# Kernel tuning notes

Hardware: AMD Instinct MI355X
Metric: run time of the kernel (lower is better)

Reference implementation:

```python
import jax, jax.numpy as jnp
import numpy as np

N_ATOMS = 50000
N_EDGES = 640000
D = 128
N_RBF = 20
N_INTER = 3

act = jax.nn.softplus


def setup_inputs() -> dict:
    key = jax.random.key(0)
    ks = jax.random.split(key, 16)
    s = 1.0 / np.sqrt(D)
    inp = {
        "x": jax.random.normal(ks[0], (N_ATOMS, D), jnp.float32),
        "g_ij": jax.random.uniform(ks[1], (N_EDGES, N_RBF), jnp.float32),
        "idx_i": jax.random.randint(ks[2], (N_EDGES,), 0, N_ATOMS),
        "idx_j": jax.random.randint(ks[3], (N_EDGES,), 0, N_ATOMS),
        "n_atoms": N_ATOMS,
        "u": jnp.ones((D,), jnp.float32),
        "Wf": jax.random.normal(ks[4], (D, D), jnp.float32) * s,
        "bf": jnp.zeros((D,), jnp.float32),
        # linear_g weight init to zero in original; use small random so grads flow
        "Wg": jax.random.normal(ks[5], (D, N_RBF), jnp.float32) * 0.01,
        "bg": jnp.zeros((D,), jnp.float32),
        "Wj": jax.random.normal(ks[6], (D, D), jnp.float32) * s,
        "bj": jnp.zeros((D,), jnp.float32),
        "Wi": jax.random.normal(ks[7], (D, D), jnp.float32) * s,
        "bi": jnp.zeros((D,), jnp.float32),
        "res_w1": jax.random.normal(ks[8], (N_INTER, D, D), jnp.float32) * s,
        "res_b1": jnp.zeros((N_INTER, D), jnp.float32),
        "res_w2": jax.random.normal(ks[9], (N_INTER, D, D), jnp.float32) * s,
        "res_b2": jnp.zeros((N_INTER, D), jnp.float32),
    }
    return inp


def reference(x, g_ij, idx_i, idx_j, n_atoms, u, Wf, bf, Wg, bg, Wj, bj, Wi, bi,
              res_w1, res_b1, res_w2, res_b2):
    x_j = x[idx_j]                                    # [E, D] gather
    xp = u * x                                        # [N, D]
    # sequential_j: act -> linear_j -> act, gated by linear_g(g_ij)
    vp = act(act(x_j) @ Wj.T + bj) * (g_ij @ Wg.T + bg)   # [E, D]
    vm = act(act(x) @ Wi.T + bi)                      # [N, D]
    v = jax.ops.segment_sum(vp, idx_i, num_segments=n_atoms) + vm
    for l in range(res_w1.shape[0]):
        h = act(v) @ res_w1[l].T + res_b1[l]
        h = act(h) @ res_w2[l].T + res_b2[l]
        v = h + v
    v = act(v)
    return xp + v @ Wf.T + bf
```

## Files before the change

kernel.cpp:

```cpp
#include <hip/hip_runtime.h>
#include <hip/hip_fp16.h>

#define DD 128

typedef __attribute__((ext_vector_type(8))) short short8;
typedef __attribute__((ext_vector_type(8))) unsigned short ushort8;
typedef __attribute__((ext_vector_type(4))) float floatx4;
typedef unsigned int uint32;

__device__ __forceinline__ float sp(float x) {
    return fmaxf(x, 0.0f) + __logf(1.0f + __expf(-fabsf(x)));
}

__device__ __forceinline__ unsigned short f2bf(float f) {
    union { float f; uint32 u; } c; c.f = f;
    const uint32 u = c.u;
    return (unsigned short)((u + 0x7fffu + ((u >> 16) & 1u)) >> 16);
}

__device__ __forceinline__ unsigned short f2h(float f) {
    __half h = __float2half(f);
    return __builtin_bit_cast(unsigned short, h);
}

__global__ __launch_bounds__(256)
void convert_w(const float* __restrict__ Wj, const float* __restrict__ Wi,
               const float* __restrict__ rw1, const float* __restrict__ rw2,
               const float* __restrict__ Wf, unsigned short* __restrict__ out,
               const float* __restrict__ g, unsigned short* __restrict__ gh,
               int gchunks)
{
    if ((int)blockIdx.x >= 72) {
        const int gid = ((int)blockIdx.x - 72) * 256 + threadIdx.x;
        if (gid < gchunks) {
            const float4 f0 = reinterpret_cast<const float4*>(g)[2 * gid];
            const float4 f1 = reinterpret_cast<const float4*>(g)[2 * gid + 1];
            ushort8 o;
            o[0] = f2h(f0.x); o[1] = f2h(f0.y); o[2] = f2h(f0.z); o[3] = f2h(f0.w);
            o[4] = f2h(f1.x); o[5] = f2h(f1.y); o[6] = f2h(f1.z); o[7] = f2h(f1.w);
            reinterpret_cast<ushort8*>(gh)[gid] = o;
        }
        return;
    }
    const int gid = blockIdx.x * 256 + threadIdx.x;
    const int mat = gid >> 11;
    const int f8  = gid & 2047;
    const float* src;
    if      (mat == 0) src = Wj;
    else if (mat == 1) src = Wi;
    else if (mat <= 4) src = rw1 + (size_t)(mat - 2) * 16384;
    else if (mat <= 7) src = rw2 + (size_t)(mat - 5) * 16384;
    else               src = Wf;
    const int row = f8 >> 4;
    const int ch  = f8 & 15;
    const float4 a = reinterpret_cast<const float4*>(src)[2 * f8];
    const float4 b = reinterpret_cast<const float4*>(src)[2 * f8 + 1];
    ushort8 u8;
    u8[0] = f2bf(a.x); u8[1] = f2bf(a.y); u8[2] = f2bf(a.z); u8[3] = f2bf(a.w);
    u8[4] = f2bf(b.x); u8[5] = f2bf(b.y); u8[6] = f2bf(b.z); u8[7] = f2bf(b.w);
    *reinterpret_cast<ushort8*>(out + (size_t)mat * 16384 + row * 128 +
                                ((ch ^ (row & 15)) << 3)) = u8;
}

__device__ __forceinline__ void stage_wb(const unsigned short* __restrict__ Wb,
                                         unsigned short* wl, int t)
{
    #pragma unroll
    for (int i = 0; i < 8; ++i) {
        const int c = t + i * 256;
        *reinterpret_cast<ushort8*>(wl + c * 8) =
            *reinterpret_cast<const ushort8*>(Wb + c * 8);
    }
}

__device__ __forceinline__ void load_afrag_act(const float* __restrict__ X,
                                               int m, int q, int n, short8 af[4])
{
    const int mm = m < n ? m : n - 1;
    const float* row = X + (size_t)mm * DD + q * 8;
    #pragma unroll
    for (int kk = 0; kk < 4; ++kk) {
        const float4 a = *reinterpret_cast<const float4*>(row + kk * 32);
        const float4 b = *reinterpret_cast<const float4*>(row + kk * 32 + 4);
        ushort8 u;
        u[0] = f2bf(sp(a.x)); u[1] = f2bf(sp(a.y)); u[2] = f2bf(sp(a.z)); u[3] = f2bf(sp(a.w));
        u[4] = f2bf(sp(b.x)); u[5] = f2bf(sp(b.y)); u[6] = f2bf(sp(b.z)); u[7] = f2bf(sp(b.w));
        af[kk] = __builtin_bit_cast(short8, u);
    }
}

__device__ __forceinline__ void mfma_gemm(const unsigned short* wl,
                                          const short8 af[4],
                                          int cl, int q, floatx4 acc[8])
{
    #pragma unroll
    for (int nt = 0; nt < 8; ++nt) {
        const int nrow = nt * 16 + cl;
        #pragma unroll
        for (int kk = 0; kk < 4; ++kk) {
            const int chs = (kk * 4 + q) ^ cl;
            const short8 bfr = *reinterpret_cast<const short8*>(wl + nrow * 128 + (chs << 3));
            acc[nt] = __builtin_amdgcn_mfma_f32_16x16x32_bf16(af[kk], bfr, acc[nt], 0, 0, 0);
        }
    }
}

__global__ __launch_bounds__(256, 4)
void dual_gemm(const float* __restrict__ x,
               const unsigned short* __restrict__ Wb,
               const float* __restrict__ bj, const float* __restrict__ bi,
               unsigned short* __restrict__ Aout, float* __restrict__ vout, int n)
{
    __shared__ __align__(16) unsigned short wl[128 * 128];
    const int t = threadIdx.x;
    const int lane = t & 63, wv = t >> 6;
    const int cl = lane & 15, q = lane >> 4;
    const int m0 = blockIdx.x * 64 + wv * 16;

    short8 af[4];
    load_afrag_act(x, m0 + cl, q, n, af);

    stage_wb(Wb, wl, t);
    __syncthreads();

    floatx4 acc[8];
    #pragma unroll
    for (int nt = 0; nt < 8; ++nt) acc[nt] = (floatx4){0.f, 0.f, 0.f, 0.f};
    mfma_gemm(wl, af, cl, q, acc);

    #pragma unroll
    for (int nt = 0; nt < 8; ++nt) {
        const int col = nt * 16 + cl;
        const float bb = bj[col];
        #pragma unroll
        for (int r = 0; r < 4; ++r) {
            const int row = m0 + q * 4 + r;
            if (row < n) Aout[(size_t)row * DD + col] = f2bf(sp(acc[nt][r] + bb));
        }
    }

    __syncthreads();
    stage_wb(Wb + 16384, wl, t);
    __syncthreads();

    #pragma unroll
    for (int nt = 0; nt < 8; ++nt) acc[nt] = (floatx4){0.f, 0.f, 0.f, 0.f};
    mfma_gemm(wl, af, cl, q, acc);

    #pragma unroll
    for (int nt = 0; nt < 8; ++nt) {
        const int col = nt * 16 + cl;
        const float bb = bi[col];
        #pragma unroll
        for (int r = 0; r < 4; ++r) {
            const int row = m0 + q * 4 + r;
            if (row < n) vout[(size_t)row * DD + col] = sp(acc[nt][r] + bb);
        }
    }
}

__global__ __launch_bounds__(256, 2)
void tail_kernel(const float* __restrict__ vin, const float* __restrict__ x,
                 const unsigned short* __restrict__ Wb,
                 const float* __restrict__ rb1, const float* __restrict__ rb2,
                 const float* __restrict__ bf, const float* __restrict__ u,
                 float* __restrict__ out, int n)
{
    __shared__ __align__(16) unsigned short wl[2][128 * 128];
    __shared__ __align__(16) unsigned short hl[64 * 128];
    const int t = threadIdx.x;
    const int lane = t & 63, wv = t >> 6;
    const int cl = lane & 15, q = lane >> 4;
    const int mb = blockIdx.x * 64;
    const int ml2 = wv * 16 + cl;

    floatx4 vac[8];
    #pragma unroll
    for (int nt = 0; nt < 8; ++nt) {
        #pragma unroll
        for (int r = 0; r < 4; ++r) {
            const int row = mb + wv * 16 + q * 4 + r;
            const int col = nt * 16 + cl;
            vac[nt][r] = (row < n) ? vin[(size_t)row * DD + col] : 0.f;
        }
    }

    short8 af[4];
    load_afrag_act(vin, mb + wv * 16 + cl, q, n, af);

    stage_wb(Wb + 2 * 16384, wl[0], t);
    __syncthreads();
    int buf = 0;

    #pragma unroll
    for (int l = 0; l < 3; ++l) {
        stage_wb(Wb + (size_t)(5 + l) * 16384, wl[buf ^ 1], t);

        if (l > 0) {
            #pragma unroll
            for (int nt = 0; nt < 8; ++nt) {
                const int col = nt * 16 + cl;
                const int ch = col >> 3;
                #pragma unroll
                for (int r = 0; r < 4; ++r) {
                    const int ml = wv * 16 + q * 4 + r;
                    hl[ml * 128 + ((ch ^ (ml & 15)) << 3) + (col & 7)] = f2bf(sp(vac[nt][r]));
                }
            }
            #pragma unroll
            for (int kk = 0; kk < 4; ++kk)
                af[kk] = *reinterpret_cast<const short8*>(hl + ml2 * 128 + (((kk * 4 + q) ^ cl) << 3));
        }

        floatx4 acc[8];
        #pragma unroll
        for (int nt = 0; nt < 8; ++nt) acc[nt] = (floatx4){0.f, 0.f, 0.f, 0.f};
        mfma_gemm(wl[buf], af, cl, q, acc);

        const float* b1 = rb1 + (size_t)l * DD;
        #pragma unroll
        for (int nt = 0; nt < 8; ++nt) {
            const int col = nt * 16 + cl;
            const int ch = col >> 3;
            const float bb = b1[col];
            #pragma unroll
            for (int r = 0; r < 4; ++r) {
                const int ml = wv * 16 + q * 4 + r;
                hl[ml * 128 + ((ch ^ (ml & 15)) << 3) + (col & 7)] = f2bf(sp(acc[nt][r] + bb));
            }
        }
        short8 af2[4];
        #pragma unroll
        for (int kk = 0; kk < 4; ++kk)
            af2[kk] = *reinterpret_cast<const short8*>(hl + ml2 * 128 + (((kk * 4 + q) ^ cl) << 3));

        __syncthreads();
        buf ^= 1;

        const int nxt = (l < 2) ? (3 + l) : 8;
        stage_wb(Wb + (size_t)nxt * 16384, wl[buf ^ 1], t);

        mfma_gemm(wl[buf], af2, cl, q, vac);
        const float* b2 = rb2 + (size_t)l * DD;
        #pragma unroll
        for (int nt = 0; nt < 8; ++nt) {
            const float bb = b2[nt * 16 + cl];
            #pragma unroll
            for (int r = 0; r < 4; ++r) vac[nt][r] += bb;
        }

        __syncthreads();
        buf ^= 1;
    }

    #pragma unroll
    for (int nt = 0; nt < 8; ++nt) {
        const int col = nt * 16 + cl;
        const int ch = col >> 3;
        #pragma unroll
        for (int r = 0; r < 4; ++r) {
            const int ml = wv * 16 + q * 4 + r;
            hl[ml * 128 + ((ch ^ (ml & 15)) << 3) + (col & 7)] = f2bf(sp(vac[nt][r]));
        }
    }
    short8 aff[4];
    #pragma unroll
    for (int kk = 0; kk < 4; ++kk)
        aff[kk] = *reinterpret_cast<const short8*>(hl + ml2 * 128 + (((kk * 4 + q) ^ cl) << 3));

    floatx4 acc[8];
    #pragma unroll
    for (int nt = 0; nt < 8; ++nt) acc[nt] = (floatx4){0.f, 0.f, 0.f, 0.f};
    mfma_gemm(wl[buf], aff, cl, q, acc);

    #pragma unroll
    for (int nt = 0; nt < 8; ++nt) {
        const int col = nt * 16 + cl;
        const float bb = bf[col];
        const float uu = u[col];
        #pragma unroll
        for (int r = 0; r < 4; ++r) {
            const int row = mb + wv * 16 + q * 4 + r;
            if (row < n)
                out[(size_t)row * DD + col] =
                    acc[nt][r] + bb + uu * x[(size_t)row * DD + col];
        }
    }
}


__global__ __launch_bounds__(256)
void hist_kernel(const int* __restrict__ idx_i, int* __restrict__ cnt, int E)
{
    const int e = blockIdx.x * 256 + threadIdx.x;
    if (e < E) atomicAdd(&cnt[idx_i[e]], 1);
}

__global__ __launch_bounds__(256)
void scan_reduce(const int* __restrict__ cnt, int* __restrict__ bsum, int n)
{
    __shared__ int wsum[4];
    const int t = threadIdx.x;
    const int lane = t & 63, wv = t >> 6;
    const int i0 = blockIdx.x * 1024 + t * 4;
    int s = 0;
    #pragma unroll
    for (int k = 0; k < 4; ++k) if (i0 + k < n) s += cnt[i0 + k];
    #pragma unroll
    for (int d = 1; d < 64; d <<= 1) s += __shfl_down(s, d, 64);
    if (lane == 0) wsum[wv] = s;
    __syncthreads();
    if (t == 0) bsum[blockIdx.x] = wsum[0] + wsum[1] + wsum[2] + wsum[3];
}

__global__ __launch_bounds__(256)
void scan_apply(const int* __restrict__ cnt, const int* __restrict__ bsum,
                int* __restrict__ off, int* __restrict__ cnt2, int n, int nb)
{
    __shared__ int wsum[4];
    const int t = threadIdx.x;
    const int lane = t & 63, wv = t >> 6;

    int bval = (lane < nb && lane < (int)blockIdx.x) ? bsum[lane] : 0;
    #pragma unroll
    for (int d = 32; d >= 1; d >>= 1) bval += __shfl_down(bval, d, 64);
    const int blk_off = __shfl(bval, 0, 64);

    const int i0 = blockIdx.x * 1024 + t * 4;
    const int v0 = (i0 + 0 < n) ? cnt[i0 + 0] : 0;
    const int v1 = (i0 + 1 < n) ? cnt[i0 + 1] : 0;
    const int v2 = (i0 + 2 < n) ? cnt[i0 + 2] : 0;
    const int v3 = (i0 + 3 < n) ? cnt[i0 + 3] : 0;
    const int s = v0 + v1 + v2 + v3;
    int incl = s;
    #pragma unroll
    for (int d = 1; d < 64; d <<= 1) {
        const int y = __shfl_up(incl, d, 64);
        if (lane >= d) incl += y;
    }
    if (lane == 63) wsum[wv] = incl;
    __syncthreads();
    int woff = blk_off;
    #pragma unroll
    for (int w = 0; w < 4; ++w) if (w < wv) woff += wsum[w];
    const int excl = woff + incl - s;
    if (i0 + 0 < n) { off[i0 + 0] = excl;                cnt2[i0 + 0] = 0; }
    if (i0 + 1 < n) { off[i0 + 1] = excl + v0;           cnt2[i0 + 1] = 0; }
    if (i0 + 2 < n) { off[i0 + 2] = excl + v0 + v1;      cnt2[i0 + 2] = 0; }
    if (i0 + 3 < n) { off[i0 + 3] = excl + v0 + v1 + v2; cnt2[i0 + 3] = 0; }
}

__global__ __launch_bounds__(256)
void scatter_kernel(const int* __restrict__ idx_i, const int* __restrict__ idx_j,
                    const int* __restrict__ off, int* __restrict__ cnt2,
                    int2* __restrict__ spair, int E)
{
    const int e = blockIdx.x * 256 + threadIdx.x;
    if (e < E) {
        const int i = idx_i[e];
        const int p = off[i] + atomicAdd(&cnt2[i], 1);
        spair[p] = make_int2(e, idx_j[e]);
    }
}

template<int GH>
__global__ __launch_bounds__(256, 4)
void agg_kernel(const int* __restrict__ off, const int* __restrict__ cnt,
                const int2* __restrict__ spair,
                const unsigned short* __restrict__ gh,
                const float* __restrict__ g,
                const float* __restrict__ Wg, const float* __restrict__ bg,
                const unsigned short* __restrict__ A, float* __restrict__ v, int N)
{
    const int t = threadIdx.x;
    const int lane = t & 63;
    const int wid0 = blockIdx.x * 4 + (t >> 6);
    const int nw   = gridDim.x * 4;
    const int d0 = lane << 1;

    const float bg0 = bg[d0], bg1 = bg[d0 + 1];

    if (GH) {
        __half2 w0h[10], w1h[10];
        #pragma unroll
        for (int k2 = 0; k2 < 10; ++k2) {
            w0h[k2] = __floats2half2_rn(Wg[d0 * 20 + 2 * k2], Wg[d0 * 20 + 2 * k2 + 1]);
            w1h[k2] = __floats2half2_rn(Wg[(d0 + 1) * 20 + 2 * k2], Wg[(d0 + 1) * 20 + 2 * k2 + 1]);
        }

        for (int i = wid0; i < N; i += nw) {
            const int beg = off[i], num = cnt[i], end = beg + num;
            float2 acc = *reinterpret_cast<const float2*>(v + (size_t)i * DD + d0);

            int p = beg;
            while (p + 4 <= end) {
                int ee[4], jj[4];
                #pragma unroll
                for (int u = 0; u < 4; ++u) {
                    const int2 pr = spair[p + u];
                    ee[u] = __builtin_amdgcn_readfirstlane(pr.x);
                    jj[u] = __builtin_amdgcn_readfirstlane(pr.y);
                }
                uint32 aa[4];
                float2 gq[4][5];
                #pragma unroll
                for (int u = 0; u < 4; ++u) {
                    aa[u] = *reinterpret_cast<const uint32*>(A + (size_t)jj[u] * DD + d0);
                    const float2* gp = reinterpret_cast<const float2*>(gh + (size_t)ee[u] * 20);
                    #pragma unroll
                    for (int q2 = 0; q2 < 5; ++q2) gq[u][q2] = gp[q2];
                }
                #pragma unroll
                for (int u = 0; u < 4; ++u) {
                    __half2 a0 = __float2half2_rn(0.f), a1 = __float2half2_rn(0.f);
                    #pragma unroll
                    for (int q2 = 0; q2 < 5; ++q2) {
                        const __half2 h0 = __builtin_bit_cast(__half2, gq[u][q2].x);
                        const __half2 h1 = __builtin_bit_cast(__half2, gq[u][q2].y);
                        a0 = __hfma2(h0, w0h[2 * q2], a0);
                        a1 = __hfma2(h0, w1h[2 * q2], a1);
                        a0 = __hfma2(h1, w0h[2 * q2 + 1], a0);
                        a1 = __hfma2(h1, w1h[2 * q2 + 1], a1);
                    }
                    const float t0 = bg0 + __low2float(a0) + __high2float(a0);
                    const float t1 = bg1 + __low2float(a1) + __high2float(a1);
                    union { uint32 u32; float f; } cx, cy;
                    cx.u32 = aa[u] << 16;
                    cy.u32 = aa[u] & 0xffff0000u;
                    acc.x = fmaf(cx.f, t0, acc.x);
                    acc.y = fmaf(cy.f, t1, acc.y);
                }
                p += 4;
            }
            for (; p < end; ++p) {
                const int2 pr = spair[p];
                const int e0 = __builtin_amdgcn_readfirstlane(pr.x);
                const int j0 = __builtin_amdgcn_readfirstlane(pr.y);
                const uint32 a0u = *reinterpret_cast<const uint32*>(A + (size_t)j0 * DD + d0);
                const float2* gp = reinterpret_cast<const float2*>(gh + (size_t)e0 * 20);
                __half2 a0 = __float2half2_rn(0.f), a1 = __float2half2_rn(0.f);
                #pragma unroll
                for (int q2 = 0; q2 < 5; ++q2) {
                    const float2 qq = gp[q2];
                    const __half2 h0 = __builtin_bit_cast(__half2, qq.x);
                    const __half2 h1 = __builtin_bit_cast(__half2, qq.y);
                    a0 = __hfma2(h0, w0h[2 * q2], a0);
                    a1 = __hfma2(h0, w1h[2 * q2], a1);
                    a0 = __hfma2(h1, w0h[2 * q2 + 1], a0);
                    a1 = __hfma2(h1, w1h[2 * q2 + 1], a1);
                }
                const float t0 = bg0 + __low2float(a0) + __high2float(a0);
                const float t1 = bg1 + __low2float(a1) + __high2float(a1);
                union { uint32 u32; float f; } cx, cy;
                cx.u32 = a0u << 16;
                cy.u32 = a0u & 0xffff0000u;
                acc.x = fmaf(cx.f, t0, acc.x);
                acc.y = fmaf(cy.f, t1, acc.y);
            }
            *reinterpret_cast<float2*>(v + (size_t)i * DD + d0) = acc;
        }
    } else {
        float2 wg01[20];
        #pragma unroll
        for (int k = 0; k < 20; ++k) {
            wg01[k].x = Wg[d0 * 20 + k];
            wg01[k].y = Wg[(d0 + 1) * 20 + k];
        }
        for (int i = wid0; i < N; i += nw) {
            const int beg = off[i], num = cnt[i], end = beg + num;
            float2 acc = *reinterpret_cast<const float2*>(v + (size_t)i * DD + d0);
            int p = beg;
            for (; p + 2 <= end; p += 2) {
                const int2 pr0 = spair[p];
                const int2 pr1 = spair[p + 1];
                const int e0 = __builtin_amdgcn_readfirstlane(pr0.x);
                const int j0 = __builtin_amdgcn_readfirstlane(pr0.y);
                const int e1 = __builtin_amdgcn_readfirstlane(pr1.x);
                const int j1 = __builtin_amdgcn_readfirstlane(pr1.y);
                const uint32 a0 = *reinterpret_cast<const uint32*>(A + (size_t)j0 * DD + d0);
                const uint32 a1 = *reinterpret_cast<const uint32*>(A + (size_t)j1 * DD + d0);
                const float4* g0p = reinterpret_cast<const float4*>(g + (size_t)e0 * 20);
                const float4* g1p = reinterpret_cast<const float4*>(g + (size_t)e1 * 20);
                float2 t0 = make_float2(bg0, bg1), t1 = make_float2(bg0, bg1);
                #pragma unroll
                for (int qq = 0; qq < 5; ++qq) {
                    const float4 p0 = g0p[qq];
                    const float4 p1 = g1p[qq];
                    t0.x = fmaf(p0.x, wg01[qq*4+0].x, t0.x); t0.y = fmaf(p0.x, wg01[qq*4+0].y, t0.y);
                    t0.x = fmaf(p0.y, wg01[qq*4+1].x, t0.x); t0.y = fmaf(p0.y, wg01[qq*4+1].y, t0.y);
                    t0.x = fmaf(p0.z, wg01[qq*4+2].x, t0.x); t0.y = fmaf(p0.z, wg01[qq*4+2].y, t0.y);
                    t0.x = fmaf(p0.w, wg01[qq*4+3].x, t0.x); t0.y = fmaf(p0.w, wg01[qq*4+3].y, t0.y);
                    t1.x = fmaf(p1.x, wg01[qq*4+0].x, t1.x); t1.y = fmaf(p1.x, wg01[qq*4+0].y, t1.y);
                    t1.x = fmaf(p1.y, wg01[qq*4+1].x, t1.x); t1.y = fmaf(p1.y, wg01[qq*4+1].y, t1.y);
                    t1.x = fmaf(p1.z, wg01[qq*4+2].x, t1.x); t1.y = fmaf(p1.z, wg01[qq*4+2].y, t1.y);
                    t1.x = fmaf(p1.w, wg01[qq*4+3].x, t1.x); t1.y = fmaf(p1.w, wg01[qq*4+3].y, t1.y);
                }
                union { uint32 u; float f; } c0x, c0y, c1x, c1y;
                c0x.u = a0 << 16; c0y.u = a0 & 0xffff0000u;
                c1x.u = a1 << 16; c1y.u = a1 & 0xffff0000u;
                acc.x = fmaf(c0x.f, t0.x, acc.x); acc.y = fmaf(c0y.f, t0.y, acc.y);
                acc.x = fmaf(c1x.f, t1.x, acc.x); acc.y = fmaf(c1y.f, t1.y, acc.y);
            }
            if (p < end) {
                const int2 pr0 = spair[p];
                const int e0 = __builtin_amdgcn_readfirstlane(pr0.x);
                const int j0 = __builtin_amdgcn_readfirstlane(pr0.y);
                const uint32 a0 = *reinterpret_cast<const uint32*>(A + (size_t)j0 * DD + d0);
                const float4* g0p = reinterpret_cast<const float4*>(g + (size_t)e0 * 20);
                float2 t0 = make_float2(bg0, bg1);
                #pragma unroll
                for (int qq = 0; qq < 5; ++qq) {
                    const float4 p0 = g0p[qq];
                    t0.x = fmaf(p0.x, wg01[qq*4+0].x, t0.x); t0.y = fmaf(p0.x, wg01[qq*4+0].y, t0.y);
                    t0.x = fmaf(p0.y, wg01[qq*4+1].x, t0.x); t0.y = fmaf(p0.y, wg01[qq*4+1].y, t0.y);
                    t0.x = fmaf(p0.z, wg01[qq*4+2].x, t0.x); t0.y = fmaf(p0.z, wg01[qq*4+2].y, t0.y);
                    t0.x = fmaf(p0.w, wg01[qq*4+3].x, t0.x); t0.y = fmaf(p0.w, wg01[qq*4+3].y, t0.y);
                }
                union { uint32 u; float f; } c0x, c0y;
                c0x.u = a0 << 16; c0y.u = a0 & 0xffff0000u;
                acc.x = fmaf(c0x.f, t0.x, acc.x); acc.y = fmaf(c0y.f, t0.y, acc.y);
            }
            *reinterpret_cast<float2*>(v + (size_t)i * DD + d0) = acc;
        }
    }
}

extern "C" void kernel_launch(void* const* d_in, const int* in_sizes, int n_in,
                              void* d_out, int out_size, void* d_ws, size_t ws_size,
                              hipStream_t stream)
{
    const float* x     = (const float*)d_in[0];
    const float* g     = (const float*)d_in[1];
    const int*   idx_i = (const int*)d_in[2];
    const int*   idx_j = (const int*)d_in[3];
    const float* u     = (const float*)d_in[5];
    const float* Wf    = (const float*)d_in[6];
    const float* bf    = (const float*)d_in[7];
    const float* Wg    = (const float*)d_in[8];
    const float* bg    = (const float*)d_in[9];
    const float* Wj    = (const float*)d_in[10];
    const float* bj    = (const float*)d_in[11];
    const float* Wi    = (const float*)d_in[12];
    const float* bi    = (const float*)d_in[13];
    const float* rw1   = (const float*)d_in[14];
    const float* rb1   = (const float*)d_in[15];
    const float* rw2   = (const float*)d_in[16];
    const float* rb2   = (const float*)d_in[17];

    const int N = in_sizes[0] / DD;
    const int E = in_sizes[2];
    float* out = (float*)d_out;

    float*          v     = (float*)d_ws;
    unsigned short* A     = (unsigned short*)(v + (size_t)N * DD);
    int*            cnt   = (int*)(A + (size_t)N * DD);
    int*            off   = cnt + N;
    int*            cnt2  = off + N;
    int*            bsum  = cnt2 + N;
    int2*           spair = (int2*)(bsum + 64);
    unsigned short* Wb    = (unsigned short*)(spair + E);
    unsigned short* gh    = Wb + 9 * 16384;

    const size_t need_gh = (size_t)((char*)(gh + (size_t)E * 20) - (char*)d_ws);
    const bool gh_ok = ws_size >= need_gh;

    dim3 blk(256);
    const int tiles    = (N + 63) / 64;
    const int eblocks  = (E + 255) / 256;
    const int sblocks  = (N + 1023) / 1024;
    const int gchunks  = gh_ok ? (E * 20) / 8 : 0;
    const int gblocks  = gh_ok ? (gchunks + 255) / 256 : 0;

    convert_w<<<72 + gblocks, blk, 0, stream>>>(Wj, Wi, rw1, rw2, Wf, Wb,
                                                g, gh, gchunks);

    hipMemsetAsync(cnt, 0, (size_t)N * sizeof(int), stream);
    hist_kernel<<<eblocks, blk, 0, stream>>>(idx_i, cnt, E);
    scan_reduce<<<sblocks, blk, 0, stream>>>(cnt, bsum, N);
    scan_apply<<<sblocks, blk, 0, stream>>>(cnt, bsum, off, cnt2, N, sblocks);
    scatter_kernel<<<eblocks, blk, 0, stream>>>(idx_i, idx_j, off, cnt2, spair, E);

    dual_gemm<<<tiles, blk, 0, stream>>>(x, Wb, bj, bi, A, v, N);

    if (gh_ok)
        agg_kernel<1><<<2048, blk, 0, stream>>>(off, cnt, spair, gh, g,
                                                Wg, bg, A, v, N);
    else
        agg_kernel<0><<<2048, blk, 0, stream>>>(off, cnt, spair, gh, g,
                                                Wg, bg, A, v, N);

    tail_kernel<<<tiles, blk, 0, stream>>>(v, x, Wb, rb1, rb2, bf, u, out, N);
}
```

Measured before the change: 243.7 us.

## Pre-pack weights in MFMA fragment order and read tail weights from global

The weight conversion kernel now writes bf16 weights directly in per-lane MFMA B-fragment order, so each lane loads one contiguous 16-byte chunk per tile. The tail kernel drops its double-buffered LDS weight staging and barriers and reads fragments straight from global/L2, which cuts LDS use and allows 4 blocks per CU instead of 2. The risk is more global/L2 traffic per block for weights that used to be reused from LDS. dual_gemm still stages the weights through LDS, now in the new linear fragment layout.

```diff
diff --git a/kernel.cpp b/kernel.cpp
--- a/kernel.cpp
+++ b/kernel.cpp
@@ -44,22 +44,24 @@
     }
     const int gid = blockIdx.x * 256 + threadIdx.x;
     const int mat = gid >> 11;
-    const int f8  = gid & 2047;
+    const int r   = gid & 2047;
+    const int ln  = r & 63;
+    const int ntkk = r >> 6;
     const float* src;
     if      (mat == 0) src = Wj;
     else if (mat == 1) src = Wi;
     else if (mat <= 4) src = rw1 + (size_t)(mat - 2) * 16384;
     else if (mat <= 7) src = rw2 + (size_t)(mat - 5) * 16384;
     else               src = Wf;
-    const int row = f8 >> 4;
-    const int ch  = f8 & 15;
-    const float4 a = reinterpret_cast<const float4*>(src)[2 * f8];
-    const float4 b = reinterpret_cast<const float4*>(src)[2 * f8 + 1];
+    const int row = (ntkk >> 2) * 16 + (ln & 15);
+    const int c0  = ((ntkk & 3) * 4 + (ln >> 4)) * 8;
+    const float* s = src + row * DD + c0;
+    const float4 a = *reinterpret_cast<const float4*>(s);
+    const float4 b = *reinterpret_cast<const float4*>(s + 4);
     ushort8 u8;
     u8[0] = f2bf(a.x); u8[1] = f2bf(a.y); u8[2] = f2bf(a.z); u8[3] = f2bf(a.w);
     u8[4] = f2bf(b.x); u8[5] = f2bf(b.y); u8[6] = f2bf(b.z); u8[7] = f2bf(b.w);
-    *reinterpret_cast<ushort8*>(out + (size_t)mat * 16384 + row * 128 +
-                                ((ch ^ (row & 15)) << 3)) = u8;
+    *reinterpret_cast<ushort8*>(out + (size_t)mat * 16384 + (size_t)r * 8) = u8;
 }
 
 __device__ __forceinline__ void stage_wb(const unsigned short* __restrict__ Wb,
@@ -89,17 +91,15 @@
     }
 }
 
-__device__ __forceinline__ void mfma_gemm(const unsigned short* wl,
-                                          const short8 af[4],
-                                          int cl, int q, floatx4 acc[8])
+__device__ __forceinline__ void mfma_gemm(const unsigned short* __restrict__ wsrc,
+                                          const short8 af[4], int lane, floatx4 acc[8])
 {
     #pragma unroll
     for (int nt = 0; nt < 8; ++nt) {
-        const int nrow = nt * 16 + cl;
         #pragma unroll
         for (int kk = 0; kk < 4; ++kk) {
-            const int chs = (kk * 4 + q) ^ cl;
-            const short8 bfr = *reinterpret_cast<const short8*>(wl + nrow * 128 + (chs << 3));
+            const short8 bfr = *reinterpret_cast<const short8*>(
+                wsrc + (size_t)(((nt * 4 + kk) << 6) + lane) * 8);
             acc[nt] = __builtin_amdgcn_mfma_f32_16x16x32_bf16(af[kk], bfr, acc[nt], 0, 0, 0);
         }
     }
@@ -126,7 +126,7 @@
     floatx4 acc[8];
     #pragma unroll
     for (int nt = 0; nt < 8; ++nt) acc[nt] = (floatx4){0.f, 0.f, 0.f, 0.f};
-    mfma_gemm(wl, af, cl, q, acc);
+    mfma_gemm(wl, af, lane, acc);
 
     #pragma unroll
     for (int nt = 0; nt < 8; ++nt) {
@@ -145,7 +145,7 @@
 
     #pragma unroll
     for (int nt = 0; nt < 8; ++nt) acc[nt] = (floatx4){0.f, 0.f, 0.f, 0.f};
-    mfma_gemm(wl, af, cl, q, acc);
+    mfma_gemm(wl, af, lane, acc);
 
     #pragma unroll
     for (int nt = 0; nt < 8; ++nt) {
@@ -159,14 +159,13 @@
     }
 }
 
-__global__ __launch_bounds__(256, 2)
+__global__ __launch_bounds__(256, 4)
 void tail_kernel(const float* __restrict__ vin, const float* __restrict__ x,
                  const unsigned short* __restrict__ Wb,
                  const float* __restrict__ rb1, const float* __restrict__ rb2,
                  const float* __restrict__ bf, const float* __restrict__ u,
                  float* __restrict__ out, int n)
 {
-    __shared__ __align__(16) unsigned short wl[2][128 * 128];
     __shared__ __align__(16) unsigned short hl[64 * 128];
     const int t = threadIdx.x;
     const int lane = t & 63, wv = t >> 6;
@@ -188,13 +187,10 @@
     short8 af[4];
     load_afrag_act(vin, mb + wv * 16 + cl, q, n, af);
 
-    stage_wb(Wb + 2 * 16384, wl[0], t);
-    __syncthreads();
-    int buf = 0;
-
     #pragma unroll
     for (int l = 0; l < 3; ++l) {
-        stage_wb(Wb + (size_t)(5 + l) * 16384, wl[buf ^ 1], t);
+        const unsigned short* W1 = Wb + (size_t)(2 + l) * 16384;
+        const unsigned short* W2 = Wb + (size_t)(5 + l) * 16384;
 
         if (l > 0) {
             #pragma unroll
@@ -215,7 +211,7 @@
         floatx4 acc[8];
         #pragma unroll
         for (int nt = 0; nt < 8; ++nt) acc[nt] = (floatx4){0.f, 0.f, 0.f, 0.f};
-        mfma_gemm(wl[buf], af, cl, q, acc);
+        mfma_gemm(W1, af, lane, acc);
 
         const float* b1 = rb1 + (size_t)l * DD;
         #pragma unroll
@@ -234,13 +230,7 @@
         for (int kk = 0; kk < 4; ++kk)
             af2[kk] = *reinterpret_cast<const short8*>(hl + ml2 * 128 + (((kk * 4 + q) ^ cl) << 3));
 
-        __syncthreads();
-        buf ^= 1;
-
-        const int nxt = (l < 2) ? (3 + l) : 8;
-        stage_wb(Wb + (size_t)nxt * 16384, wl[buf ^ 1], t);
-
-        mfma_gemm(wl[buf], af2, cl, q, vac);
+        mfma_gemm(W2, af2, lane, vac);
         const float* b2 = rb2 + (size_t)l * DD;
         #pragma unroll
         for (int nt = 0; nt < 8; ++nt) {
@@ -248,9 +238,6 @@
             #pragma unroll
             for (int r = 0; r < 4; ++r) vac[nt][r] += bb;
         }
-
-        __syncthreads();
-        buf ^= 1;
     }
 
     #pragma unroll
@@ -271,7 +258,7 @@
     floatx4 acc[8];
     #pragma unroll
     for (int nt = 0; nt < 8; ++nt) acc[nt] = (floatx4){0.f, 0.f, 0.f, 0.f};
-    mfma_gemm(wl[buf], aff, cl, q, acc);
+    mfma_gemm(Wb + (size_t)8 * 16384, aff, lane, acc);
 
     #pragma unroll
     for (int nt = 0; nt < 8; ++nt) {
```

Result: slower. 257.9 us (+5.9%).
